# Performance work log

Measured on AMD Instinct MI355X. Metric: run time of the kernel, lower is better.

## Reference

```python
import jax, jax.numpy as jnp
import numpy as np

IN_C, OUT_C = 64, 128
HID = OUT_C // 4  # 32
NEG = 0.1  # LeakyReLU slope inside MLPs


def _leaky(x, slope):
    return jnp.where(x >= 0, x, slope * x)


def gather_neighbors(x, idx):
    # x: [B,N,F], idx: [B,N',K] -> [B,N',K,F]
    return jax.vmap(lambda xb, ib: xb[ib])(x, idx)


def setup_inputs() -> dict:
    key = jax.random.key(0)
    ks = jax.random.split(key, 12)
    B, N, K = 2, 65536, 16
    x = jax.random.normal(ks[0], (B, N, IN_C), dtype=jnp.float32)
    pos = jax.random.uniform(ks[1], (B, N, 3), dtype=jnp.float32)
    neighbor_idx = jax.random.randint(ks[2], (B, N, K), 0, N)
    s = lambda fi, fo: 1.0 / np.sqrt(fi)
    W_in = jax.random.normal(ks[3], (IN_C, HID), dtype=jnp.float32) * s(IN_C, HID)
    b_in = jnp.zeros((HID,), jnp.float32)
    Wa = jax.random.normal(ks[4], (3, HID), dtype=jnp.float32) * s(3, HID)
    ba = jnp.zeros((HID,), jnp.float32)
    Wb = jax.random.normal(ks[5], (HID, HID), dtype=jnp.float32) * s(HID, HID)
    bb = jnp.zeros((HID,), jnp.float32)
    W_out = jax.random.normal(ks[6], (HID, OUT_C), dtype=jnp.float32) * s(HID, OUT_C)
    b_out = jnp.zeros((OUT_C,), jnp.float32)
    W_sc = jax.random.normal(ks[7], (IN_C, OUT_C), dtype=jnp.float32) * s(IN_C, OUT_C)
    b_sc = jnp.zeros((OUT_C,), jnp.float32)
    return dict(x=x, pos=pos, neighbor_idx=neighbor_idx,
                W_in=W_in, b_in=b_in, Wa=Wa, ba=ba, Wb=Wb, bb=bb,
                W_out=W_out, b_out=b_out, W_sc=W_sc, b_sc=b_sc)


def reference(x, pos, neighbor_idx, W_in, b_in, Wa, ba, Wb, bb, W_out, b_out, W_sc, b_sc):
    # shortcut (in_channels != out_channels -> Linear)
    residual = x @ W_sc + b_sc                      # [B,N,OUT]
    h = _leaky(x @ W_in + b_in, NEG)                # [B,N,HID]
    # PointConv: per-edge weights from relative positions
    nbr_pos = gather_neighbors(pos, neighbor_idx)   # [B,N,K,3]
    rel = pos[:, :, None, :] - nbr_pos              # [B,N,K,3]
    w = _leaky(rel @ Wa + ba, NEG) @ Wb + bb        # [B,N,K,HID]
    hg = gather_neighbors(h, neighbor_idx)          # [B,N,K,HID]
    conv = jnp.sum(w * hg, axis=2)                  # [B,N,HID]
    out = conv @ W_out + b_out                      # [B,N,OUT]
    return _leaky(out + residual, 0.01)             # F.leaky_relu default slope
```

## Files before the change

kernel.cpp:

```cpp
#include <hip/hip_runtime.h>
#include <hip/hip_bf16.h>

#define IN_C 64
#define OUT_C 128
#define HID 32
#define KNB 16

typedef __attribute__((ext_vector_type(8))) short short8;
typedef __attribute__((ext_vector_type(4))) float f32x4;

__device__ __forceinline__ float leaky(float v, float s) { return fmaxf(v, s * v); }

__device__ __forceinline__ unsigned bf16u(float f) {
    __hip_bfloat16 h = __float2bfloat16(f);
    return (unsigned)*reinterpret_cast<unsigned short*>(&h);
}
__device__ __forceinline__ short bf16s(float f) {
    __hip_bfloat16 h = __float2bfloat16(f);
    return *reinterpret_cast<short*>(&h);
}

__global__ __launch_bounds__(256) void hid_mfma(
    const float* __restrict__ x, const float* __restrict__ Win,
    const float* __restrict__ bin, const float* __restrict__ pos,
    const float* __restrict__ Wout, const float* __restrict__ Wsc,
    unsigned* __restrict__ h2, float4* __restrict__ pos4,
    short* __restrict__ pk, int P)
{
    int tg = blockIdx.x * 256 + (int)threadIdx.x;

    if (tg < P) {
        float4 v;
        v.x = pos[3L * tg + 0]; v.y = pos[3L * tg + 1];
        v.z = pos[3L * tg + 2]; v.w = 0.f;
        pos4[tg] = v;
    }
    if (tg < 1536) {
        int ks = tg >> 9, rem = tg & 511;
        int nt = rem >> 6, g2 = (rem >> 4) & 3, n2 = rem & 15;
        int col = nt * 16 + n2;
        short8 v;
        #pragma unroll
        for (int e = 0; e < 8; ++e) {
            int row = ks * 32 + 8 * g2 + e;
            float f = (row < 32) ? Wout[row * OUT_C + col]
                                 : Wsc[(row - 32) * OUT_C + col];
            v[e] = bf16s(f);
        }
        *(short8*)(pk + (long)tg * 8) = v;
    }

    int lane = threadIdx.x & 63;
    int widx = __builtin_amdgcn_readfirstlane(threadIdx.x >> 6);
    int wavebase = (blockIdx.x * 4 + widx) * 16;
    if (wavebase >= P) return;
    int n = lane & 15, g = lane >> 4;

    short8 bfr[2][2];
    #pragma unroll
    for (int ks = 0; ks < 2; ++ks)
        #pragma unroll
        for (int nt = 0; nt < 2; ++nt)
            #pragma unroll
            for (int e = 0; e < 8; ++e)
                bfr[ks][nt][e] = bf16s(Win[(ks * 32 + 8 * g + e) * HID + nt * 16 + n]);

    float bv0 = bin[n], bv1 = bin[16 + n];

    const float* xr = x + (long)(wavebase + n) * IN_C;
    short8 a[2];
    #pragma unroll
    for (int ks = 0; ks < 2; ++ks) {
        float4 v0 = *(const float4*)(xr + ks * 32 + 8 * g);
        float4 v1 = *(const float4*)(xr + ks * 32 + 8 * g + 4);
        a[ks][0] = bf16s(v0.x); a[ks][1] = bf16s(v0.y);
        a[ks][2] = bf16s(v0.z); a[ks][3] = bf16s(v0.w);
        a[ks][4] = bf16s(v1.x); a[ks][5] = bf16s(v1.y);
        a[ks][6] = bf16s(v1.z); a[ks][7] = bf16s(v1.w);
    }

    f32x4 acc0 = { bv0, bv0, bv0, bv0 };
    f32x4 acc1 = { bv1, bv1, bv1, bv1 };
    acc0 = __builtin_amdgcn_mfma_f32_16x16x32_bf16(a[0], bfr[0][0], acc0, 0, 0, 0);
    acc0 = __builtin_amdgcn_mfma_f32_16x16x32_bf16(a[1], bfr[1][0], acc0, 0, 0, 0);
    acc1 = __builtin_amdgcn_mfma_f32_16x16x32_bf16(a[0], bfr[0][1], acc1, 0, 0, 0);
    acc1 = __builtin_amdgcn_mfma_f32_16x16x32_bf16(a[1], bfr[1][1], acc1, 0, 0, 0);

    #pragma unroll
    for (int r = 0; r < 4; ++r) {
        unsigned lo = bf16u(leaky(acc0[r], 0.1f));
        unsigned hi = bf16u(leaky(acc1[r], 0.1f));
        h2[(long)(wavebase + 4 * g + r) * 16 + n] = (hi << 16) | lo;
    }
}

__global__ __launch_bounds__(128) __attribute__((amdgpu_waves_per_eu(1, 4)))
void edgeout_mfma(
    const float* __restrict__ x, const float4* __restrict__ pos4,
    const int* __restrict__ nbr, const unsigned* __restrict__ h2,
    const float* __restrict__ Wa, const float* __restrict__ ba,
    const float* __restrict__ Wb, const float* __restrict__ bb,
    const short* __restrict__ pk, const float* __restrict__ bout,
    const float* __restrict__ bsc, float* __restrict__ out,
    int N, int P, int nblk)
{
    __shared__ float cbuf[2][32 * 17];

    int cpx = nblk >> 3;
    int ebid = (blockIdx.x & 7) * cpx + (blockIdx.x >> 3);

    int tid = threadIdx.x;
    int lane = tid & 63;
    int widx = __builtin_amdgcn_readfirstlane(tid >> 6);
    int n = lane & 15, g = lane >> 4;
    int wavebase = (ebid * 2 + widx) * 16;
    if (wavebase >= P) return;
    long pbase = (wavebase >= N) ? (long)N : 0;

    float waX[8], waY[8], waZ[8], bav[8];
    #pragma unroll
    for (int e = 0; e < 8; ++e) {
        int k = 8 * g + e;
        waX[e] = Wa[k]; waY[e] = Wa[HID + k]; waZ[e] = Wa[2 * HID + k];
        bav[e] = ba[k];
    }
    short8 wb0, wb1;
    #pragma unroll
    for (int e = 0; e < 8; ++e) {
        int k = 8 * g + e;
        wb0[e] = bf16s(Wb[k * HID + n]);
        wb1[e] = bf16s(Wb[k * HID + 16 + n]);
    }
    float bb0 = bb[n], bb1 = bb[16 + n];
    float* cb = cbuf[widx];

    const float* xr = x + (long)(wavebase + n) * IN_C;
    float4 u0 = *(const float4*)(xr + 8 * g);
    float4 u1 = *(const float4*)(xr + 8 * g + 4);
    float4 u2 = *(const float4*)(xr + 32 + 8 * g);
    float4 u3 = *(const float4*)(xr + 32 + 8 * g + 4);

    f32x4 cacc0 = { 0.f, 0.f, 0.f, 0.f };
    f32x4 cacc1 = { 0.f, 0.f, 0.f, 0.f };

    int4  qv[KNB]; int qs[KNB];
    float4 pp[KNB], pq[KNB];
    unsigned hv[KNB][4];

#define IDX(i) {                                                        \
        const int* nr = nbr + (long)(wavebase + (i)) * KNB;             \
        qv[i] = *(const int4*)(nr + 4 * g);                             \
        qs[i] = nr[n]; }
#define GATHER(i) {                                                     \
        pp[i] = pos4[wavebase + (i)];                                   \
        pq[i] = pos4[pbase + qs[i]];                                    \
        hv[i][0] = h2[(pbase + qv[i].x) * 16 + n];                      \
        hv[i][1] = h2[(pbase + qv[i].y) * 16 + n];                      \
        hv[i][2] = h2[(pbase + qv[i].z) * 16 + n];                      \
        hv[i][3] = h2[(pbase + qv[i].w) * 16 + n]; }

    #pragma unroll
    for (int pt = 0; pt < KNB; ++pt) {
        if (pt == 0) { IDX(0) IDX(1) IDX(2) GATHER(0) GATHER(1) }
        if (pt + 3 < KNB) IDX(pt + 3)
        if (pt + 2 < KNB) GATHER(pt + 2)

        float rx = pp[pt].x - pq[pt].x;
        float ry = pp[pt].y - pq[pt].y;
        float rz = pp[pt].z - pq[pt].z;

        short8 af;
        #pragma unroll
        for (int e = 0; e < 8; ++e) {
            float tv = fmaf(rx, waX[e], fmaf(ry, waY[e], fmaf(rz, waZ[e], bav[e])));
            af[e] = bf16s(leaky(tv, 0.1f));
        }

        f32x4 w0 = { bb0, bb0, bb0, bb0 };
        f32x4 w1 = { bb1, bb1, bb1, bb1 };
        w0 = __builtin_amdgcn_mfma_f32_16x16x32_bf16(af, wb0, w0, 0, 0, 0);
        w1 = __builtin_amdgcn_mfma_f32_16x16x32_bf16(af, wb1, w1, 0, 0, 0);

        float hA0 = __uint_as_float(hv[pt][0] << 16), hB0 = __uint_as_float(hv[pt][0] & 0xffff0000u);
        float hA1 = __uint_as_float(hv[pt][1] << 16), hB1 = __uint_as_float(hv[pt][1] & 0xffff0000u);
        float hA2 = __uint_as_float(hv[pt][2] << 16), hB2 = __uint_as_float(hv[pt][2] & 0xffff0000u);
        float hA3 = __uint_as_float(hv[pt][3] << 16), hB3 = __uint_as_float(hv[pt][3] & 0xffff0000u);

        short8 am0 = { bf16s(w0[0] * hA0), bf16s(w0[1] * hA1),
                       bf16s(w0[2] * hA2), bf16s(w0[3] * hA3), 0, 0, 0, 0 };
        short8 am1 = { bf16s(w1[0] * hB0), bf16s(w1[1] * hB1),
                       bf16s(w1[2] * hB2), bf16s(w1[3] * hB3), 0, 0, 0, 0 };

        short sv = (n == pt) ? (short)0x3F80 : (short)0;
        short8 bsel = { sv, sv, sv, sv, 0, 0, 0, 0 };

        cacc0 = __builtin_amdgcn_mfma_f32_16x16x32_bf16(am0, bsel, cacc0, 0, 0, 0);
        cacc1 = __builtin_amdgcn_mfma_f32_16x16x32_bf16(am1, bsel, cacc1, 0, 0, 0);
    }
#undef IDX
#undef GATHER

    #pragma unroll
    for (int r = 0; r < 4; ++r) {
        cb[(4 * g + r) * 17 + n]      = cacc0[r];
        cb[(16 + 4 * g + r) * 17 + n] = cacc1[r];
    }
    asm volatile("s_waitcnt lgkmcnt(0)" ::: "memory");

    short8 a0, a1, a2;
    #pragma unroll
    for (int e = 0; e < 8; ++e)
        a0[e] = bf16s(cb[(8 * g + e) * 17 + n]);
    a1[0] = bf16s(u0.x); a1[1] = bf16s(u0.y); a1[2] = bf16s(u0.z); a1[3] = bf16s(u0.w);
    a1[4] = bf16s(u1.x); a1[5] = bf16s(u1.y); a1[6] = bf16s(u1.z); a1[7] = bf16s(u1.w);
    a2[0] = bf16s(u2.x); a2[1] = bf16s(u2.y); a2[2] = bf16s(u2.z); a2[3] = bf16s(u2.w);
    a2[4] = bf16s(u3.x); a2[5] = bf16s(u3.y); a2[6] = bf16s(u3.z); a2[7] = bf16s(u3.w);

    #pragma unroll 2
    for (int nt = 0; nt < 8; ++nt) {
        short8 b0 = *(const short8*)(pk + ((long)(0 * 8 + nt) * 64 + lane) * 8);
        short8 b1 = *(const short8*)(pk + ((long)(1 * 8 + nt) * 64 + lane) * 8);
        short8 b2 = *(const short8*)(pk + ((long)(2 * 8 + nt) * 64 + lane) * 8);
        int o = nt * 16 + n;
        float bv = bout[o] + bsc[o];
        f32x4 acc = { bv, bv, bv, bv };
        acc = __builtin_amdgcn_mfma_f32_16x16x32_bf16(a0, b0, acc, 0, 0, 0);
        acc = __builtin_amdgcn_mfma_f32_16x16x32_bf16(a1, b1, acc, 0, 0, 0);
        acc = __builtin_amdgcn_mfma_f32_16x16x32_bf16(a2, b2, acc, 0, 0, 0);
        #pragma unroll
        for (int r = 0; r < 4; ++r)
            out[(long)(wavebase + 4 * g + r) * OUT_C + o] = leaky(acc[r], 0.01f);
    }
}

extern "C" void kernel_launch(void* const* d_in, const int* in_sizes, int n_in,
                              void* d_out, int out_size, void* d_ws, size_t ws_size,
                              hipStream_t stream) {
    const float* x    = (const float*)d_in[0];
    const float* pos  = (const float*)d_in[1];
    const int*   nbr  = (const int*)d_in[2];
    const float* Win  = (const float*)d_in[3];
    const float* bin  = (const float*)d_in[4];
    const float* Wa   = (const float*)d_in[5];
    const float* ba   = (const float*)d_in[6];
    const float* Wb   = (const float*)d_in[7];
    const float* bb   = (const float*)d_in[8];
    const float* Wout = (const float*)d_in[9];
    const float* bout = (const float*)d_in[10];
    const float* Wsc  = (const float*)d_in[11];
    const float* bsc  = (const float*)d_in[12];
    float* out = (float*)d_out;

    int P = in_sizes[0] / IN_C;
    int N = P / 2;

    unsigned* h2  = (unsigned*)d_ws;
    float4*  pos4 = (float4*)((char*)d_ws + (size_t)P * 64);
    short*   pk   = (short*)((char*)d_ws + (size_t)P * 64 + (size_t)P * 16);

    hid_mfma<<<(P + 63) / 64, 256, 0, stream>>>(
        x, Win, bin, pos, Wout, Wsc, h2, pos4, pk, P);
    int nblk = (P + 31) / 32;
    edgeout_mfma<<<nblk, 128, 0, stream>>>(
        x, pos4, nbr, h2, Wa, ba, Wb, bb, pk, bout, bsc, out, N, P, nblk);
}
```

Baseline: 62.55 us.

## Precompute fp16 relative positions per edge in a separate kernel

Adds a new kernel that computes every edge's relative position (center minus neighbor), stores it as packed fp16 short4, and removes the pos4 repacking from hid_mfma. The edge kernel then reads one coalesced 8-byte value per edge instead of doing two float4 pos gathers, one of them random. This costs an extra launch and an extra write and read of P*16*8 bytes, and the relative positions lose precision by going to fp16.

```diff
diff --git a/kernel.cpp b/kernel.cpp
--- a/kernel.cpp
+++ b/kernel.cpp
@@ -1,5 +1,6 @@
 #include <hip/hip_runtime.h>
 #include <hip/hip_bf16.h>
+#include <hip/hip_fp16.h>
 
 #define IN_C 64
 #define OUT_C 128
@@ -19,22 +20,40 @@
     __hip_bfloat16 h = __float2bfloat16(f);
     return *reinterpret_cast<short*>(&h);
 }
+__device__ __forceinline__ short f16bits(float f) {
+    __half h = __float2half(f);
+    return *reinterpret_cast<short*>(&h);
+}
+__device__ __forceinline__ float f16val(short s) {
+    __half h; *reinterpret_cast<short*>(&h) = s;
+    return __half2float(h);
+}
+
+__global__ __launch_bounds__(256) void rel_kernel(
+    const float* __restrict__ pos, const int* __restrict__ nbr,
+    short4* __restrict__ rel4, int N, int P)
+{
+    int tg = blockIdx.x * 256 + (int)threadIdx.x;
+    if (tg >= P * KNB) return;
+    int p = tg >> 4;
+    long pbase = (p >= N) ? (long)N : 0;
+    long q = pbase + nbr[tg];
+    float rx = pos[3L * p + 0] - pos[3 * q + 0];
+    float ry = pos[3L * p + 1] - pos[3 * q + 1];
+    float rz = pos[3L * p + 2] - pos[3 * q + 2];
+    short4 v;
+    v.x = f16bits(rx); v.y = f16bits(ry); v.z = f16bits(rz); v.w = 0;
+    rel4[tg] = v;
+}
 
 __global__ __launch_bounds__(256) void hid_mfma(
     const float* __restrict__ x, const float* __restrict__ Win,
-    const float* __restrict__ bin, const float* __restrict__ pos,
+    const float* __restrict__ bin,
     const float* __restrict__ Wout, const float* __restrict__ Wsc,
-    unsigned* __restrict__ h2, float4* __restrict__ pos4,
-    short* __restrict__ pk, int P)
+    unsigned* __restrict__ h2, short* __restrict__ pk, int P)
 {
     int tg = blockIdx.x * 256 + (int)threadIdx.x;
 
-    if (tg < P) {
-        float4 v;
-        v.x = pos[3L * tg + 0]; v.y = pos[3L * tg + 1];
-        v.z = pos[3L * tg + 2]; v.w = 0.f;
-        pos4[tg] = v;
-    }
     if (tg < 1536) {
         int ks = tg >> 9, rem = tg & 511;
         int nt = rem >> 6, g2 = (rem >> 4) & 3, n2 = rem & 15;
@@ -96,7 +115,7 @@
 
 __global__ __launch_bounds__(128) __attribute__((amdgpu_waves_per_eu(1, 4)))
 void edgeout_mfma(
-    const float* __restrict__ x, const float4* __restrict__ pos4,
+    const float* __restrict__ x, const short4* __restrict__ rel4,
     const int* __restrict__ nbr, const unsigned* __restrict__ h2,
     const float* __restrict__ Wa, const float* __restrict__ ba,
     const float* __restrict__ Wb, const float* __restrict__ bb,
@@ -143,17 +162,14 @@
     f32x4 cacc0 = { 0.f, 0.f, 0.f, 0.f };
     f32x4 cacc1 = { 0.f, 0.f, 0.f, 0.f };
 
-    int4  qv[KNB]; int qs[KNB];
-    float4 pp[KNB], pq[KNB];
+    int4  qv[KNB];
+    short4 rl[KNB];
     unsigned hv[KNB][4];
 
 #define IDX(i) {                                                        \
-        const int* nr = nbr + (long)(wavebase + (i)) * KNB;             \
-        qv[i] = *(const int4*)(nr + 4 * g);                             \
-        qs[i] = nr[n]; }
+        qv[i] = *(const int4*)(nbr + (long)(wavebase + (i)) * KNB + 4 * g); }
 #define GATHER(i) {                                                     \
-        pp[i] = pos4[wavebase + (i)];                                   \
-        pq[i] = pos4[pbase + qs[i]];                                    \
+        rl[i] = rel4[(long)(wavebase + (i)) * KNB + n];                 \
         hv[i][0] = h2[(pbase + qv[i].x) * 16 + n];                      \
         hv[i][1] = h2[(pbase + qv[i].y) * 16 + n];                      \
         hv[i][2] = h2[(pbase + qv[i].z) * 16 + n];                      \
@@ -165,9 +181,9 @@
         if (pt + 3 < KNB) IDX(pt + 3)
         if (pt + 2 < KNB) GATHER(pt + 2)
 
-        float rx = pp[pt].x - pq[pt].x;
-        float ry = pp[pt].y - pq[pt].y;
-        float rz = pp[pt].z - pq[pt].z;
+        float rx = f16val(rl[pt].x);
+        float ry = f16val(rl[pt].y);
+        float rz = f16val(rl[pt].z);
 
         short8 af;
         #pragma unroll
@@ -254,13 +270,13 @@
     int P = in_sizes[0] / IN_C;
     int N = P / 2;
 
-    unsigned* h2  = (unsigned*)d_ws;
-    float4*  pos4 = (float4*)((char*)d_ws + (size_t)P * 64);
-    short*   pk   = (short*)((char*)d_ws + (size_t)P * 64 + (size_t)P * 16);
-
-    hid_mfma<<<(P + 63) / 64, 256, 0, stream>>>(
-        x, Win, bin, pos, Wout, Wsc, h2, pos4, pk, P);
+    unsigned* h2   = (unsigned*)d_ws;
+    short4*   rel4 = (short4*)((char*)d_ws + (size_t)P * 64);
+    short*    pk   = (short*)((char*)d_ws + (size_t)P * 64 + (size_t)P * KNB * 8);
+
+    rel_kernel<<<(P * KNB + 255) / 256, 256, 0, stream>>>(pos, nbr, rel4, N, P);
+    hid_mfma<<<(P + 63) / 64, 256, 0, stream>>>(x, Win, bin, Wout, Wsc, h2, pk, P);
     int nblk = (P + 31) / 32;
     edgeout_mfma<<<nblk, 128, 0, stream>>>(
-        x, pos4, nbr, h2, Wa, ba, Wb, bb, pk, bout, bsc, out, N, P, nblk);
-}
+        x, rel4, nbr, h2, Wa, ba, Wb, bb, pk, bout, bsc, out, N, P, nblk);
+}
```

New measurement: 73.71 us. 17.9% more time.

## Prefetch neighbor positions once per wave and distribute relative offsets via shuffles

Applied to the files above, without the earlier changes.

Moves the per-point neighbor-position gathers out of the pipelined loop. Each lane now loads one of the wave's 256 neighbor indices and its position up front, computes the relative offset, packs it as fp16, and lanes fetch their values with cross-lane shuffles inside the loop. This cuts the redundant pos4 gathers that were repeated for each of the four lane groups and frees registers from the pp/pq/qs arrays. In exchange it adds shuffle instructions per iteration and rounds relative positions to fp16 before the position MLP.

```diff
diff --git a/kernel.cpp b/kernel.cpp
--- a/kernel.cpp
+++ b/kernel.cpp
@@ -1,5 +1,6 @@
 #include <hip/hip_runtime.h>
 #include <hip/hip_bf16.h>
+#include <hip/hip_fp16.h>
 
 #define IN_C 64
 #define OUT_C 128
@@ -18,6 +19,14 @@
 __device__ __forceinline__ short bf16s(float f) {
     __hip_bfloat16 h = __float2bfloat16(f);
     return *reinterpret_cast<short*>(&h);
+}
+__device__ __forceinline__ unsigned f16b(float f) {
+    __half h = __float2half(f);
+    return (unsigned)*reinterpret_cast<unsigned short*>(&h);
+}
+__device__ __forceinline__ float f16val(unsigned s) {
+    __half h; *reinterpret_cast<unsigned short*>(&h) = (unsigned short)s;
+    return __half2float(h);
 }
 
 __global__ __launch_bounds__(256) void hid_mfma(
@@ -117,6 +126,17 @@
     if (wavebase >= P) return;
     long pbase = (wavebase >= N) ? (long)N : 0;
 
+    const int* nb = nbr + (long)wavebase * KNB;
+    int q0 = nb[lane], q1 = nb[64 + lane], q2 = nb[128 + lane], q3 = nb[192 + lane];
+    float4 pq0 = pos4[pbase + q0];
+    float4 pq1 = pos4[pbase + q1];
+    float4 pq2 = pos4[pbase + q2];
+    float4 pq3 = pos4[pbase + q3];
+    float4 po0 = pos4[wavebase + g];
+    float4 po1 = pos4[wavebase + 4 + g];
+    float4 po2 = pos4[wavebase + 8 + g];
+    float4 po3 = pos4[wavebase + 12 + g];
+
     float waX[8], waY[8], waZ[8], bav[8];
     #pragma unroll
     for (int e = 0; e < 8; ++e) {
@@ -140,20 +160,25 @@
     float4 u2 = *(const float4*)(xr + 32 + 8 * g);
     float4 u3 = *(const float4*)(xr + 32 + 8 * g + 4);
 
+    int relA[4], relB[4];
+    relA[0] = (int)(f16b(po0.x - pq0.x) | (f16b(po0.y - pq0.y) << 16));
+    relB[0] = (int)f16b(po0.z - pq0.z);
+    relA[1] = (int)(f16b(po1.x - pq1.x) | (f16b(po1.y - pq1.y) << 16));
+    relB[1] = (int)f16b(po1.z - pq1.z);
+    relA[2] = (int)(f16b(po2.x - pq2.x) | (f16b(po2.y - pq2.y) << 16));
+    relB[2] = (int)f16b(po2.z - pq2.z);
+    relA[3] = (int)(f16b(po3.x - pq3.x) | (f16b(po3.y - pq3.y) << 16));
+    relB[3] = (int)f16b(po3.z - pq3.z);
+
     f32x4 cacc0 = { 0.f, 0.f, 0.f, 0.f };
     f32x4 cacc1 = { 0.f, 0.f, 0.f, 0.f };
 
-    int4  qv[KNB]; int qs[KNB];
-    float4 pp[KNB], pq[KNB];
+    int4 qv[KNB];
     unsigned hv[KNB][4];
 
 #define IDX(i) {                                                        \
-        const int* nr = nbr + (long)(wavebase + (i)) * KNB;             \
-        qv[i] = *(const int4*)(nr + 4 * g);                             \
-        qs[i] = nr[n]; }
+        qv[i] = *(const int4*)(nbr + (long)(wavebase + (i)) * KNB + 4 * g); }
 #define GATHER(i) {                                                     \
-        pp[i] = pos4[wavebase + (i)];                                   \
-        pq[i] = pos4[pbase + qs[i]];                                    \
         hv[i][0] = h2[(pbase + qv[i].x) * 16 + n];                      \
         hv[i][1] = h2[(pbase + qv[i].y) * 16 + n];                      \
         hv[i][2] = h2[(pbase + qv[i].z) * 16 + n];                      \
@@ -165,9 +190,12 @@
         if (pt + 3 < KNB) IDX(pt + 3)
         if (pt + 2 < KNB) GATHER(pt + 2)
 
-        float rx = pp[pt].x - pq[pt].x;
-        float ry = pp[pt].y - pq[pt].y;
-        float rz = pp[pt].z - pq[pt].z;
+        int src = ((pt & 3) << 4) + n;
+        unsigned da = (unsigned)__shfl(relA[pt >> 2], src, 64);
+        unsigned db = (unsigned)__shfl(relB[pt >> 2], src, 64);
+        float rx = f16val(da & 0xffffu);
+        float ry = f16val(da >> 16);
+        float rz = f16val(db & 0xffffu);
 
         short8 af;
         #pragma unroll
```

Measured after the change: 65.94 us. 1.05x slower.
